# Kernel tuning notes

Hardware: AMD Instinct MI355X
Metric: run time of the kernel (lower is better)

## Reference

```python
import jax, jax.numpy as jnp
import numpy as np

K = 11          # kernel_size
SIGMA = 1.5
CH = 3          # image channels


def _gaussian_kernel(ch):
    coords = jnp.arange(K, dtype=jnp.float32) - (K - 1) / 2
    g = jnp.exp(-coords ** 2 / (2 * SIGMA ** 2))
    g = g / g.sum()
    k2d = jnp.outer(g, g)                       # [K, K]
    return jnp.tile(k2d[None, None], (ch, 1, 1, 1))  # [C, 1, K, K] depthwise


def setup_inputs() -> dict:
    key = jax.random.key(0)
    kx, ky = jax.random.split(key)
    x = jax.random.normal(kx, (32, CH, 512, 512), dtype=jnp.float32)
    y = jax.random.normal(ky, (32, CH, 512, 512), dtype=jnp.float32)
    kernel = _gaussian_kernel(CH)
    return {"x": x, "y": y, "kernel": kernel}


def _blur(v, kernel):
    # depthwise 2D Gaussian blur, SAME padding (K odd)
    c = v.shape[1]
    pad = K // 2
    return jax.lax.conv_general_dilated(
        v, kernel, window_strides=(1, 1), padding=[(pad, pad), (pad, pad)],
        dimension_numbers=("NCHW", "OIHW", "NCHW"), feature_group_count=c)


def reference(x, y, kernel):
    C1 = 0.01 ** 2
    C2 = 0.03 ** 2
    mu_x = _blur(x, kernel)
    mu_y = _blur(y, kernel)
    sigma_x = _blur(x * x, kernel) - mu_x ** 2
    sigma_y = _blur(y * y, kernel) - mu_y ** 2
    sigma_xy = _blur(x * y, kernel) - mu_x * mu_y
    ssim_num = (2 * mu_x * mu_y + C1) * (2 * sigma_xy + C2)
    ssim_den = (mu_x ** 2 + mu_y ** 2 + C1) * (sigma_x + sigma_y + C2)
    ssim = ssim_num / (ssim_den + 1e-8)
    return ((1.0 - ssim) / 2.0).mean()
```

## Files before the change

### kernel.cpp

```cpp
#include <hip/hip_runtime.h>
#include <hip/hip_bf16.h>

#define IMG    512
#define KSZ    11
#define HALO   5
#define STRIP  64
#define PANEL  16
#define WPS    84
#define WRSZ   (24 * WPS)

typedef short bf16x8 __attribute__((ext_vector_type(8)));
typedef float f32x4  __attribute__((ext_vector_type(4)));
union S8 { bf16x8 v; ushort u16[8]; uint u32[4]; };

__device__ __forceinline__ uint cvtpk(float lo, float hi) {
    uint r;
    asm("v_cvt_pk_bf16_f32 %0, %1, %2" : "=v"(r) : "v"(lo), "v"(hi));
    return r;
}
__device__ __forceinline__ float2 pk_mul(float2 a, float2 b) {
    float2 d;
    asm("v_pk_mul_f32 %0, %1, %2" : "=v"(d) : "v"(a), "v"(b));
    return d;
}
__device__ __forceinline__ ushort f2bf(float f) {
    union { __hip_bfloat16 h; ushort u; } c;
    c.h = __float2bfloat16(f);
    return c.u;
}


__global__ __launch_bounds__(256)
void dssim_mfma_kernel(const float* __restrict__ x,
                       const float* __restrict__ y,
                       const float* __restrict__ kern,
                       float* __restrict__ out)
{
    __shared__ float  sgf[16];
    __shared__ ushort gext[64];
    __shared__ uint   Wring[4 * WRSZ];
    __shared__ float  wsum[4];

    const int tid = threadIdx.x;
    const int l   = tid & 63;
    const int wv  = tid >> 6;
    const int q   = l >> 4;
    const int cj  = l & 15;
    const int wb  = wv * WRSZ;

    if (tid < KSZ) {
        float s = 0.f;
        #pragma unroll
        for (int j = 0; j < KSZ; ++j) s += kern[tid * KSZ + j];
        sgf[tid] = s;
    }
    for (int i = l; i < 3 * WPS; i += 64) Wring[wb + i] = 0u;
    __syncthreads();
    if (tid < 64) {
        const int d = tid - 18;
        gext[tid] = (d >= 0 && d < KSZ) ? f2bf(sgf[d]) : (ushort)0;
    }
    __syncthreads();

    S8 tgh, tgv;
    #pragma unroll
    for (int ii = 0; ii < 8; ++ii) {
        tgh.u16[ii] = gext[15 + q * 8 + ii - cj];
        tgv.u16[ii] = gext[17 + q * 8 + ii - cj];
    }

    const int plane  = blockIdx.z;
    const int half   = blockIdx.y;
    const int cstrip = blockIdx.x * STRIP;
    const int base   = plane * (IMG * IMG);

    const int  cb    = cstrip - 8 + 16 * wv + 8 * q;
    const bool colok = (cb >= 0) && (cb + 8 <= IMG);
    const float* xp  = x + base + cb;
    const float* yp  = y + base + cb;

    const int t0   = half ? 15 : 0;
    const int t1   = half ? 32 : 16;
    const int vmin = half ? 17 : 1;

    f32x4 xa, xb, ya, yb;
    auto load8 = [&](int t) {
        const int r = t * PANEL + cj;
        if (r < IMG && colok) {
            const float* px = xp + r * IMG;
            const float* py = yp + r * IMG;
            xa = *(const f32x4*)px;  xb = *(const f32x4*)(px + 4);
            ya = *(const f32x4*)py;  yb = *(const f32x4*)(py + 4);
        } else {
            const f32x4 zz = {0.f, 0.f, 0.f, 0.f};
            xa = zz; xb = zz; ya = zz; yb = zz;
        }
    };

    load8(t0);

    const f32x4 z0 = {0.f, 0.f, 0.f, 0.f};
    const float C1 = 1e-4f, C2 = 9e-4f;
    float local = 0.f;
    int hb = (8 * t0) % 24;

    for (int t = t0; t <= t1; ++t) {
        float2 x01 = {xa[0], xa[1]}, x23 = {xa[2], xa[3]};
        float2 x45 = {xb[0], xb[1]}, x67 = {xb[2], xb[3]};
        float2 y01 = {ya[0], ya[1]}, y23 = {ya[2], ya[3]};
        float2 y45 = {yb[0], yb[1]}, y67 = {yb[2], yb[3]};
        S8 fx, fy, fxx, fyy, fxy;
        #pragma unroll
        for (int w = 0; w < 4; ++w) {
            const float2 xv = (w == 0) ? x01 : (w == 1) ? x23 : (w == 2) ? x45 : x67;
            const float2 yv = (w == 0) ? y01 : (w == 1) ? y23 : (w == 2) ? y45 : y67;
            const float2 xxv = pk_mul(xv, xv);
            const float2 yyv = pk_mul(yv, yv);
            const float2 xyv = pk_mul(xv, yv);
            fx .u32[w] = cvtpk(xv.x,  xv.y);
            fy .u32[w] = cvtpk(yv.x,  yv.y);
            fxx.u32[w] = cvtpk(xxv.x, xxv.y);
            fyy.u32[w] = cvtpk(yyv.x, yyv.y);
            fxy.u32[w] = cvtpk(xyv.x, xyv.y);
        }

        if (t < t1) load8(t + 1);

        {
            int p0 = hb + 2 * q + 3;  if (p0 >= 24) p0 -= 24;
            int p1 = p0 + 1;          if (p1 >= 24) p1 -= 24;
            const int rw0 = wb + p0 * WPS + cj;
            const int rw1 = wb + p1 * WPS + cj;
            f32x4 d;
            d = __builtin_amdgcn_mfma_f32_16x16x32_bf16(fx.v,  tgh.v, z0, 0, 0, 0);
            Wring[rw0 +  0] = cvtpk(d[0], d[1]);
            Wring[rw1 +  0] = cvtpk(d[2], d[3]);
            d = __builtin_amdgcn_mfma_f32_16x16x32_bf16(fy.v,  tgh.v, z0, 0, 0, 0);
            Wring[rw0 + 16] = cvtpk(d[0], d[1]);
            Wring[rw1 + 16] = cvtpk(d[2], d[3]);
            d = __builtin_amdgcn_mfma_f32_16x16x32_bf16(fxx.v, tgh.v, z0, 0, 0, 0);
            Wring[rw0 + 32] = cvtpk(d[0], d[1]);
            Wring[rw1 + 32] = cvtpk(d[2], d[3]);
            d = __builtin_amdgcn_mfma_f32_16x16x32_bf16(fyy.v, tgh.v, z0, 0, 0, 0);
            Wring[rw0 + 48] = cvtpk(d[0], d[1]);
            Wring[rw1 + 48] = cvtpk(d[2], d[3]);
            d = __builtin_amdgcn_mfma_f32_16x16x32_bf16(fxy.v, tgh.v, z0, 0, 0, 0);
            Wring[rw0 + 64] = cvtpk(d[0], d[1]);
            Wring[rw1 + 64] = cvtpk(d[2], d[3]);
        }

        if (t >= vmin) {
            const int vb = (hb >= 8) ? hb - 8 : hb + 16;
            int vr[4];
            #pragma unroll
            for (int ii = 0; ii < 4; ++ii) {
                int pp = vb + 4 * q + ii;  if (pp >= 24) pp -= 24;
                vr[ii] = wb + pp * WPS + cj;
            }
            f32x4 vf[5];
            #pragma unroll
            for (int f = 0; f < 5; ++f) {
                S8 b;
                #pragma unroll
                for (int ii = 0; ii < 4; ++ii) b.u32[ii] = Wring[vr[ii] + f * 16];
                vf[f] = __builtin_amdgcn_mfma_f32_16x16x32_bf16(tgv.v, b.v, z0, 0, 0, 0);
            }
            #pragma unroll
            for (int r = 0; r < 4; ++r) {
                const float mx  = vf[0][r], my  = vf[1][r];
                const float exx = vf[2][r], eyy = vf[3][r], exy = vf[4][r];
                const float sxv = fmaf(-mx, mx, exx);
                const float syv = fmaf(-my, my, eyy);
                const float sxy = fmaf(-mx, my, exy);
                const float num = fmaf(2.f, mx * my, C1) * fmaf(2.f, sxy, C2);
                const float den = fmaf(mx, mx, fmaf(my, my, C1)) * (sxv + syv + C2);
                const float ssim = __fdividef(num, den + 1e-8f);
                local += (1.f - ssim) * 0.5f;
            }
        }

        hb += 8;  if (hb >= 24) hb -= 24;
    }

    #pragma unroll
    for (int o = 32; o > 0; o >>= 1) local += __shfl_down(local, o, 64);
    if (l == 0) wsum[wv] = local;
    __syncthreads();
    if (tid == 0) {
        const float s = wsum[0] + wsum[1] + wsum[2] + wsum[3];
        atomicAdd(out, s * (1.f / 25165824.f));
    }
}

extern "C" void kernel_launch(void* const* d_in, const int* in_sizes, int n_in,
                              void* d_out, int out_size, void* d_ws, size_t ws_size,
                              hipStream_t stream)
{
    const float* x    = (const float*)d_in[0];
    const float* y    = (const float*)d_in[1];
    const float* kern = (const float*)d_in[2];
    float* out = (float*)d_out;

    hipMemsetAsync(out, 0, sizeof(float), stream);

    dim3 grid(IMG / STRIP, 2, 32 * 3);
    dssim_mfma_kernel<<<grid, 256, 0, stream>>>(x, y, kern, out);
}
```

Measured before the change: 82.97 us.

## Deepen software pipeline: two-panel prefetch and vertical pass lagging by two steps

Grows the LDS ring from 24 to 32 panel slots so indices wrap with a power-of-two mask instead of compare-and-subtract. The main loop now double-buffers global loads two panels ahead and runs the vertical MFMA pass two steps behind the horizontal pass. Each vertical pass is also moved ahead of the horizontal write in the step. This is meant to hide global load latency and LDS write-to-read dependencies, at the cost of more registers and LDS and one extra loop iteration.

```diff
diff --git a/kernel.cpp b/kernel.cpp
--- a/kernel.cpp
+++ b/kernel.cpp
@@ -7,7 +7,8 @@
 #define STRIP  64
 #define PANEL  16
 #define WPS    84
-#define WRSZ   (24 * WPS)
+#define NPAIR  32
+#define WRSZ   (NPAIR * WPS)
 
 typedef short bf16x8 __attribute__((ext_vector_type(8)));
 typedef float f32x4  __attribute__((ext_vector_type(4)));
@@ -80,11 +81,18 @@
     const float* yp  = y + base + cb;
 
     const int t0   = half ? 15 : 0;
-    const int t1   = half ? 32 : 16;
-    const int vmin = half ? 17 : 1;
-
-    f32x4 xa, xb, ya, yb;
-    auto load8 = [&](int t) {
+    const int t1   = half ? 33 : 17;
+    const int hmax = half ? 32 : 16;
+    const int vmin = half ? 18 : 2;
+
+    const f32x4 z0 = {0.f, 0.f, 0.f, 0.f};
+    const float C1 = 1e-4f, C2 = 9e-4f;
+    float local = 0.f;
+    int hb = (8 * t0) & 31;
+
+    f32x4 xa0, xb0, ya0, yb0, xa1, xb1, ya1, yb1;
+
+    auto load8 = [&](int t, f32x4& xa, f32x4& xb, f32x4& ya, f32x4& yb) {
         const int r = t * PANEL + cj;
         if (r < IMG && colok) {
             const float* px = xp + r * IMG;
@@ -92,43 +100,63 @@
             xa = *(const f32x4*)px;  xb = *(const f32x4*)(px + 4);
             ya = *(const f32x4*)py;  yb = *(const f32x4*)(py + 4);
         } else {
-            const f32x4 zz = {0.f, 0.f, 0.f, 0.f};
-            xa = zz; xb = zz; ya = zz; yb = zz;
+            xa = z0; xb = z0; ya = z0; yb = z0;
         }
     };
 
-    load8(t0);
-
-    const f32x4 z0 = {0.f, 0.f, 0.f, 0.f};
-    const float C1 = 1e-4f, C2 = 9e-4f;
-    float local = 0.f;
-    int hb = (8 * t0) % 24;
-
-    for (int t = t0; t <= t1; ++t) {
-        float2 x01 = {xa[0], xa[1]}, x23 = {xa[2], xa[3]};
-        float2 x45 = {xb[0], xb[1]}, x67 = {xb[2], xb[3]};
-        float2 y01 = {ya[0], ya[1]}, y23 = {ya[2], ya[3]};
-        float2 y45 = {yb[0], yb[1]}, y67 = {yb[2], yb[3]};
-        S8 fx, fy, fxx, fyy, fxy;
-        #pragma unroll
-        for (int w = 0; w < 4; ++w) {
-            const float2 xv = (w == 0) ? x01 : (w == 1) ? x23 : (w == 2) ? x45 : x67;
-            const float2 yv = (w == 0) ? y01 : (w == 1) ? y23 : (w == 2) ? y45 : y67;
-            const float2 xxv = pk_mul(xv, xv);
-            const float2 yyv = pk_mul(yv, yv);
-            const float2 xyv = pk_mul(xv, yv);
-            fx .u32[w] = cvtpk(xv.x,  xv.y);
-            fy .u32[w] = cvtpk(yv.x,  yv.y);
-            fxx.u32[w] = cvtpk(xxv.x, xxv.y);
-            fyy.u32[w] = cvtpk(yyv.x, yyv.y);
-            fxy.u32[w] = cvtpk(xyv.x, xyv.y);
+    auto step = [&](int t, f32x4& xa, f32x4& xb, f32x4& ya, f32x4& yb) {
+        if (t >= vmin) {
+            const int vb = hb ^ 16;
+            int vr[4];
+            #pragma unroll
+            for (int ii = 0; ii < 4; ++ii)
+                vr[ii] = wb + ((vb + 4 * q + ii) & 31) * WPS + cj;
+            f32x4 vf[5];
+            #pragma unroll
+            for (int f = 0; f < 5; ++f) {
+                S8 b;
+                #pragma unroll
+                for (int ii = 0; ii < 4; ++ii) b.u32[ii] = Wring[vr[ii] + f * 16];
+                vf[f] = __builtin_amdgcn_mfma_f32_16x16x32_bf16(tgv.v, b.v, z0, 0, 0, 0);
+            }
+            #pragma unroll
+            for (int r = 0; r < 4; ++r) {
+                const float mx  = vf[0][r], my  = vf[1][r];
+                const float exx = vf[2][r], eyy = vf[3][r], exy = vf[4][r];
+                const float sxv = fmaf(-mx, mx, exx);
+                const float syv = fmaf(-my, my, eyy);
+                const float sxy = fmaf(-mx, my, exy);
+                const float num = fmaf(2.f, mx * my, C1) * fmaf(2.f, sxy, C2);
+                const float den = fmaf(mx, mx, fmaf(my, my, C1)) * (sxv + syv + C2);
+                const float ssim = __fdividef(num, den + 1e-8f);
+                local += (1.f - ssim) * 0.5f;
+            }
         }
 
-        if (t < t1) load8(t + 1);
-
-        {
-            int p0 = hb + 2 * q + 3;  if (p0 >= 24) p0 -= 24;
-            int p1 = p0 + 1;          if (p1 >= 24) p1 -= 24;
+        if (t <= hmax) {
+            float2 x01 = {xa[0], xa[1]}, x23 = {xa[2], xa[3]};
+            float2 x45 = {xb[0], xb[1]}, x67 = {xb[2], xb[3]};
+            float2 y01 = {ya[0], ya[1]}, y23 = {ya[2], ya[3]};
+            float2 y45 = {yb[0], yb[1]}, y67 = {yb[2], yb[3]};
+            S8 fx, fy, fxx, fyy, fxy;
+            #pragma unroll
+            for (int w = 0; w < 4; ++w) {
+                const float2 xv = (w == 0) ? x01 : (w == 1) ? x23 : (w == 2) ? x45 : x67;
+                const float2 yv = (w == 0) ? y01 : (w == 1) ? y23 : (w == 2) ? y45 : y67;
+                const float2 xxv = pk_mul(xv, xv);
+                const float2 yyv = pk_mul(yv, yv);
+                const float2 xyv = pk_mul(xv, yv);
+                fx .u32[w] = cvtpk(xv.x,  xv.y);
+                fy .u32[w] = cvtpk(yv.x,  yv.y);
+                fxx.u32[w] = cvtpk(xxv.x, xxv.y);
+                fyy.u32[w] = cvtpk(yyv.x, yyv.y);
+                fxy.u32[w] = cvtpk(xyv.x, xyv.y);
+            }
+
+            if (t + 2 <= hmax) load8(t + 2, xa, xb, ya, yb);
+
+            const int p0  = (hb + 2 * q + 3) & 31;
+            const int p1  = (p0 + 1) & 31;
             const int rw0 = wb + p0 * WPS + cj;
             const int rw1 = wb + p1 * WPS + cj;
             f32x4 d;
@@ -149,37 +177,15 @@
             Wring[rw1 + 64] = cvtpk(d[2], d[3]);
         }
 
-        if (t >= vmin) {
-            const int vb = (hb >= 8) ? hb - 8 : hb + 16;
-            int vr[4];
-            #pragma unroll
-            for (int ii = 0; ii < 4; ++ii) {
-                int pp = vb + 4 * q + ii;  if (pp >= 24) pp -= 24;
-                vr[ii] = wb + pp * WPS + cj;
-            }
-            f32x4 vf[5];
-            #pragma unroll
-            for (int f = 0; f < 5; ++f) {
-                S8 b;
-                #pragma unroll
-                for (int ii = 0; ii < 4; ++ii) b.u32[ii] = Wring[vr[ii] + f * 16];
-                vf[f] = __builtin_amdgcn_mfma_f32_16x16x32_bf16(tgv.v, b.v, z0, 0, 0, 0);
-            }
-            #pragma unroll
-            for (int r = 0; r < 4; ++r) {
-                const float mx  = vf[0][r], my  = vf[1][r];
-                const float exx = vf[2][r], eyy = vf[3][r], exy = vf[4][r];
-                const float sxv = fmaf(-mx, mx, exx);
-                const float syv = fmaf(-my, my, eyy);
-                const float sxy = fmaf(-mx, my, exy);
-                const float num = fmaf(2.f, mx * my, C1) * fmaf(2.f, sxy, C2);
-                const float den = fmaf(mx, mx, fmaf(my, my, C1)) * (sxv + syv + C2);
-                const float ssim = __fdividef(num, den + 1e-8f);
-                local += (1.f - ssim) * 0.5f;
-            }
-        }
-
-        hb += 8;  if (hb >= 24) hb -= 24;
+        hb = (hb + 8) & 31;
+    };
+
+    load8(t0,     xa0, xb0, ya0, yb0);
+    load8(t0 + 1, xa1, xb1, ya1, yb1);
+
+    for (int tt = t0; tt <= t1; tt += 2) {
+        step(tt, xa0, xb0, ya0, yb0);
+        if (tt + 1 <= t1) step(tt + 1, xa1, xb1, ya1, yb1);
     }
 
     #pragma unroll
```

Result: faster. 76.24 us (-8.1%).
